# Kernel tuning notes

Measured on AMD Instinct MI355X. Metric: run time of the kernel, lower is better.

Reference implementation:

```python
import jax, jax.numpy as jnp
import numpy as np

NEG_INF = -1e30  # mask value used by QANet's apply_mask


def setup_inputs() -> dict:
    key = jax.random.key(0)
    ks = jax.random.split(key, 6)
    B, C, Q, H = 64, 1024, 128, 512
    return {
        "x_context": jax.random.normal(ks[0], (B, C, H), dtype=jnp.float32),
        "x_query": jax.random.normal(ks[1], (B, Q, H), dtype=jnp.float32),
        "context_mask": jnp.ones((B, C), dtype=jnp.float32),
        "query_mask": jnp.ones((B, Q), dtype=jnp.float32),
        "W0": jax.random.normal(ks[2], (H,), dtype=jnp.float32) * 0.05,
        "W1": jax.random.normal(ks[3], (H,), dtype=jnp.float32) * 0.05,
        "W2": jax.random.normal(ks[4], (H,), dtype=jnp.float32) * 0.05,
        "bias": jnp.zeros((1,), dtype=jnp.float32),
    }


def reference(x_context, x_query, context_mask, query_mask, W0, W1, W2, bias):
    # Trilinear similarity S[b,c,q] = q.W0 + c.W1 + (q*W2).c + bias
    # (original computes [B,Q,C] then transposes; we build [B,C,Q] directly)
    sub0 = jnp.einsum('bqh,h->bq', x_query, W0)          # [B,Q]
    sub1 = jnp.einsum('bch,h->bc', x_context, W1)        # [B,C]
    sub2 = jnp.einsum('bch,bqh->bcq', x_context, x_query * W2)  # [B,C,Q]
    S = sub2 + sub1[:, :, None] + sub0[:, None, :] + bias  # [B,C,Q]

    mq = query_mask[:, None, :]    # [B,1,Q]
    mc = context_mask[:, :, None]  # [B,C,1]

    # context-to-query: softmax over query axis, masked by query_mask
    S_ = jax.nn.softmax(S + (1.0 - mq) * NEG_INF, axis=-1)  # [B,C,Q]
    c2q = jnp.einsum('bcq,bqh->bch', S_, x_query)           # [B,C,H]

    # query-to-context: softmax over context axis, masked by context_mask
    S_c = jax.nn.softmax(S + (1.0 - mc) * NEG_INF, axis=1)  # [B,C,Q]
    S_T = jnp.swapaxes(S_c, 1, 2)                            # [B,Q,C]
    # (S_ @ S_T) @ x_context, associated as S_ @ (S_T @ x_context)
    tmp = jnp.einsum('bqc,bch->bqh', S_T, x_context)        # [B,Q,H]
    q2c = jnp.einsum('bcq,bqh->bch', S_, tmp)               # [B,C,H]
    return c2q, q2c
```

## Files before the change

kernel.cpp:

```cpp
#include <hip/hip_runtime.h>

#define BB 64
#define CC 1024
#define QQ 128
#define HH 512

typedef short bf16x8 __attribute__((ext_vector_type(8)));
typedef float f32x4 __attribute__((ext_vector_type(4)));

#define GLD16(g, l)                                                            \
    __builtin_amdgcn_global_load_lds(                                          \
        (const __attribute__((address_space(1))) unsigned int*)(g),            \
        (__attribute__((address_space(3))) unsigned int*)(l), 16, 0, 0)

__device__ __forceinline__ unsigned short f2bf(float f) {
    unsigned u = __float_as_uint(f);
    u += 0x7FFF + ((u >> 16) & 1);
    return (unsigned short)(u >> 16);
}
__device__ __forceinline__ unsigned pk2(float lo, float hi) {
    return (unsigned)f2bf(lo) | ((unsigned)f2bf(hi) << 16);
}

__device__ __forceinline__ unsigned xcd_swz(unsigned orig, unsigned nwg) {
    return (orig & 7u) * (nwg >> 3) + (orig >> 3);
}

__global__ __launch_bounds__(256) void k_sub0(const float* __restrict__ xq,
                                              const float* __restrict__ w0,
                                              float* __restrict__ sub0,
                                              float* __restrict__ colsum) {
    if (blockIdx.x < 32) colsum[blockIdx.x * 256 + threadIdx.x] = 0.0f;
    int wave = threadIdx.x >> 6;
    int lane = threadIdx.x & 63;
    int row  = blockIdx.x * 4 + wave;
    const float* p = xq + (size_t)row * HH + lane * 8;
    float4 a0 = *(const float4*)(p);
    float4 a1 = *(const float4*)(p + 4);
    float4 b0 = *(const float4*)(w0 + lane * 8);
    float4 b1 = *(const float4*)(w0 + lane * 8 + 4);
    float s = a0.x*b0.x + a0.y*b0.y + a0.z*b0.z + a0.w*b0.w
            + a1.x*b1.x + a1.y*b1.y + a1.z*b1.z + a1.w*b1.w;
    #pragma unroll
    for (int off = 32; off; off >>= 1) s += __shfl_xor(s, off);
    if (lane == 0) sub0[row] = s;
}

__global__ __launch_bounds__(256) void k_prep(const float* __restrict__ xq,
                                              const float* __restrict__ w2,
                                              const float* __restrict__ qmask,
                                              unsigned short* __restrict__ xqw2b,
                                              unsigned short* __restrict__ xqmT) {
    int b  = blockIdx.y;
    int ht = blockIdx.x * 128;
    int tid = threadIdx.x;
    __shared__ __align__(16) unsigned short sT[128][132];

    {
        int q  = tid >> 1;
        int hh = (tid & 1) * 64;
        float qm = qmask[b * QQ + q];
        const float* xp = xq + ((size_t)b * QQ + q) * HH + ht + hh;
        unsigned short* wr = xqw2b + ((size_t)b * QQ + q) * HH + ht + hh;
        #pragma unroll
        for (int i = 0; i < 16; i++) {
            float4 v = *(const float4*)(xp + i * 4);
            float4 w = *(const float4*)(w2 + ht + hh + i * 4);
            uint2 pw; pw.x = pk2(v.x * w.x, v.y * w.y);
                      pw.y = pk2(v.z * w.z, v.w * w.w);
            *(uint2*)(wr + i * 4) = pw;
            uint2 pm; pm.x = pk2(v.x * qm, v.y * qm);
                      pm.y = pk2(v.z * qm, v.w * qm);
            *(uint2*)(&sT[q][hh + i * 4]) = pm;
        }
    }
    __syncthreads();
    {
        int h  = tid >> 1;
        int qh = (tid & 1) * 64;
        unsigned short* orow = xqmT + ((size_t)b * HH + ht + h) * QQ + qh;
        #pragma unroll
        for (int i = 0; i < 8; i++) {
            uint4 o;
            o.x = (unsigned)sT[qh + i*8 + 0][h] | ((unsigned)sT[qh + i*8 + 1][h] << 16);
            o.y = (unsigned)sT[qh + i*8 + 2][h] | ((unsigned)sT[qh + i*8 + 3][h] << 16);
            o.z = (unsigned)sT[qh + i*8 + 4][h] | ((unsigned)sT[qh + i*8 + 5][h] << 16);
            o.w = (unsigned)sT[qh + i*8 + 6][h] | ((unsigned)sT[qh + i*8 + 7][h] << 16);
            *(uint4*)(orow + i * 8) = o;
        }
    }
}

__global__ __launch_bounds__(256) void k_scores(
    const float* __restrict__ xc, const unsigned short* __restrict__ xqw2b,
    const float* __restrict__ w1, const float* __restrict__ cmask,
    const float* __restrict__ qmask, const float* __restrict__ bias,
    const float* __restrict__ sub0, unsigned short* __restrict__ Ebf,
    float* __restrict__ rowsum, float* __restrict__ colsum) {
    unsigned swz = xcd_swz(blockIdx.x, CC / 64 * BB);
    int b  = swz >> 4;
    int c0 = (swz & 15) * 64;
    int tid  = threadIdx.x;
    int lane = tid & 63, wave = tid >> 6;
    int quad = lane >> 4, lcol = lane & 15;
    int wrow = (wave >> 1) * 32, wcol = (wave & 1) * 64;

    __shared__ __align__(16) unsigned short sA[2][64][32];
    __shared__ __align__(16) unsigned short sB[2][128][32];
    __shared__ float sW1[512];
    __shared__ float sSub1[64];
    __shared__ float sS0[128], sQm[128], sCm[64];
    __shared__ float sRowP[2][64], sColP[2][128];

    sW1[tid] = w1[tid]; sW1[tid + 256] = w1[tid + 256];
    if (tid < 128) {
        sS0[tid] = sub0[b * QQ + tid] + bias[0];
        sQm[tid] = qmask[b * QQ + tid];
    }
    if (tid < 64) sCm[tid] = cmask[b * CC + c0 + tid];

    f32x4 acc[2][4];
    #pragma unroll
    for (int i = 0; i < 2; i++)
        #pragma unroll
        for (int j = 0; j < 4; j++) acc[i][j] = (f32x4)0.0f;
    float s1 = 0.0f;

    int arow = tid >> 2, akh = (tid & 3) * 8;
    const float* gbase = xc + ((size_t)(b * CC + c0 + arow)) * HH + akh;

    __syncthreads();

    {
        float4 v0 = *(const float4*)(gbase);
        float4 v1 = *(const float4*)(gbase + 4);
        const float* wp = sW1 + akh;
        s1 += v0.x*wp[0] + v0.y*wp[1] + v0.z*wp[2] + v0.w*wp[3]
            + v1.x*wp[4] + v1.y*wp[5] + v1.z*wp[6] + v1.w*wp[7];
        uint4 p;
        p.x = pk2(v0.x, v0.y); p.y = pk2(v0.z, v0.w);
        p.z = pk2(v1.x, v1.y); p.w = pk2(v1.z, v1.w);
        *(uint4*)&sA[0][arow][akh] = p;
    }
    #pragma unroll
    for (int j = 0; j < 2; j++) {
        int chunk = wave * 2 + j;
        int row = chunk * 16 + (lane >> 2);
        GLD16(xqw2b + ((size_t)b * QQ + row) * HH + (lane & 3) * 8,
              (unsigned short*)sB[0] + chunk * 512);
    }
    __syncthreads();

    for (int t = 0; t < 16; ++t) {
        int cur = t & 1, alt = cur ^ 1;
        bool pf = (t < 15);
        int kn = (t + 1) * 32;
        float4 v0, v1;
        if (pf) {
            const float* gp = gbase + kn;
            v0 = *(const float4*)(gp);
            v1 = *(const float4*)(gp + 4);
            #pragma unroll
            for (int j = 0; j < 2; j++) {
                int chunk = wave * 2 + j;
                int row = chunk * 16 + (lane >> 2);
                GLD16(xqw2b + ((size_t)b * QQ + row) * HH + kn + (lane & 3) * 8,
                      (unsigned short*)sB[alt] + chunk * 512);
            }
        }
        bf16x8 af[2];
        #pragma unroll
        for (int mi = 0; mi < 2; mi++)
            af[mi] = *(const bf16x8*)&sA[cur][wrow + mi * 16 + lcol][quad * 8];
        #pragma unroll
        for (int ni = 0; ni < 4; ni++) {
            bf16x8 bfr = *(const bf16x8*)&sB[cur][wcol + ni * 16 + lcol][quad * 8];
            #pragma unroll
            for (int mi = 0; mi < 2; mi++)
                acc[mi][ni] = __builtin_amdgcn_mfma_f32_16x16x32_bf16(
                    af[mi], bfr, acc[mi][ni], 0, 0, 0);
        }
        if (pf) {
            const float* wp = sW1 + kn + akh;
            s1 += v0.x*wp[0] + v0.y*wp[1] + v0.z*wp[2] + v0.w*wp[3]
                + v1.x*wp[4] + v1.y*wp[5] + v1.z*wp[6] + v1.w*wp[7];
            uint4 p;
            p.x = pk2(v0.x, v0.y); p.y = pk2(v0.z, v0.w);
            p.z = pk2(v1.x, v1.y); p.w = pk2(v1.z, v1.w);
            *(uint4*)&sA[alt][arow][akh] = p;
        }
        __syncthreads();
    }

    s1 += __shfl_xor(s1, 1);
    s1 += __shfl_xor(s1, 2);
    if ((tid & 3) == 0) sSub1[arow] = s1;
    __syncthreads();

    float rsp[2][4];
    float csp[4] = {0.f, 0.f, 0.f, 0.f};
    #pragma unroll
    for (int mi = 0; mi < 2; mi++)
        #pragma unroll
        for (int r = 0; r < 4; r++) rsp[mi][r] = 0.f;

    #pragma unroll
    for (int mi = 0; mi < 2; mi++) {
        #pragma unroll
        for (int ni = 0; ni < 4; ni++) {
            int col = wcol + ni * 16 + lcol;
            float qm = sQm[col], s0 = sS0[col];
            #pragma unroll
            for (int r = 0; r < 4; r++) {
                int row = wrow + mi * 16 + quad * 4 + r;
                float e = __expf(acc[mi][ni][r] + sSub1[row] + s0);
                acc[mi][ni][r] = e;
                rsp[mi][r] += e * qm;
                csp[ni] += e * sCm[row];
            }
        }
    }
    #pragma unroll
    for (int mi = 0; mi < 2; mi++)
        #pragma unroll
        for (int r = 0; r < 4; r++) {
            float v = rsp[mi][r];
            v += __shfl_xor(v, 1); v += __shfl_xor(v, 2);
            v += __shfl_xor(v, 4); v += __shfl_xor(v, 8);
            if (lcol == 0) sRowP[wave & 1][wrow + mi * 16 + quad * 4 + r] = v;
        }
    #pragma unroll
    for (int ni = 0; ni < 4; ni++) {
        float v = csp[ni];
        v += __shfl_xor(v, 16); v += __shfl_xor(v, 32);
        if (quad == 0) sColP[wave >> 1][wcol + ni * 16 + lcol] = v;
    }
    #pragma unroll
    for (int mi = 0; mi < 2; mi++)
        #pragma unroll
        for (int ni = 0; ni < 4; ni++) {
            int col = wcol + ni * 16 + lcol;
            #pragma unroll
            for (int r = 0; r < 4; r++) {
                int row = wrow + mi * 16 + quad * 4 + r;
                Ebf[((size_t)(b * CC + c0 + row)) * QQ + col] = f2bf(acc[mi][ni][r]);
            }
        }
    __syncthreads();
    if (tid < 64)
        rowsum[(size_t)b * CC + c0 + tid] = sRowP[0][tid] + sRowP[1][tid];
    if (tid < 128)
        atomicAdd(&colsum[b * QQ + tid], sColP[0][tid] + sColP[1][tid]);
}

__global__ __launch_bounds__(256) void k_tmp(
    const unsigned short* __restrict__ Ebf, const float* __restrict__ xc,
    const float* __restrict__ cmask, const float* __restrict__ qmask,
    const float* __restrict__ colsum, unsigned short* __restrict__ tmpT) {
    unsigned swz = xcd_swz(blockIdx.x, HH / 64 * BB);
    int b  = swz >> 3;
    int h0 = (swz & 7) * 64;
    int tid  = threadIdx.x;
    int lane = tid & 63, wave = tid >> 6;
    int quad = lane >> 4, lcol = lane & 15;
    int wrow = (wave >> 1) * 64;
    int wcol = (wave & 1) * 32;

    __shared__ __align__(16) unsigned int sAu[2][128 * 16];
    __shared__ __align__(16) unsigned int sBu[2][64 * 16];
    __shared__ float sInv[128];
    if (tid < 128) sInv[tid] = qmask[b * QQ + tid] / colsum[b * QQ + tid];

    f32x4 acc[4][2];
    #pragma unroll
    for (int i = 0; i < 4; i++) { acc[i][0] = (f32x4)0.f; acc[i][1] = (f32x4)0.f; }

    int tp = tid >> 4;
    int tq = tid & 15;

    const unsigned short* ebase = Ebf + ((size_t)b * CC + 2 * tp) * QQ + tq * 8;
    const float*          xbase = xc  + ((size_t)b * CC + 2 * tp) * HH + h0 + tq * 4;
    const float*          mbase = cmask + (size_t)b * CC + 2 * tp;

    {
        union { uint4 v; unsigned short s[8]; } r0, r1;
        r0.v = *(const uint4*)(ebase);
        r1.v = *(const uint4*)(ebase + QQ);
        float cm0 = mbase[0];
        float cm1 = mbase[1];
        float4 f0 = *(const float4*)(xbase);
        float4 f1 = *(const float4*)(xbase + HH);
        #pragma unroll
        for (int j = 0; j < 8; j++) {
            int q = tq * 8 + j;
            unsigned pk = (unsigned)r0.s[j] | ((unsigned)r1.s[j] << 16);
            sAu[0][q * 16 + (((tp >> 2) ^ (q >> 3 & 3)) << 2) + (tp & 3)] = pk;
        }
        float a0[4] = {f0.x, f0.y, f0.z, f0.w};
        float a1[4] = {f1.x, f1.y, f1.z, f1.w};
        #pragma unroll
        for (int j = 0; j < 4; j++) {
            int h = tq * 4 + j;
            unsigned pk = pk2(a0[j] * cm0, a1[j] * cm1);
            sBu[0][h * 16 + (((tp >> 2) ^ (h >> 3 & 3)) << 2) + (tp & 3)] = pk;
        }
    }
    __syncthreads();

    for (int t = 0; t < 32; ++t) {
        int cur = t & 1, alt = cur ^ 1;
        bool pf = (t < 31);
        int cn = (t + 1) * 32;
        union { uint4 v; unsigned short s[8]; } r0, r1;
        float4 f0, f1;
        float cm0, cm1;
        if (pf) {
            r0.v = *(const uint4*)(ebase + (size_t)cn * QQ);
            r1.v = *(const uint4*)(ebase + (size_t)cn * QQ + QQ);
            cm0 = mbase[cn];
            cm1 = mbase[cn + 1];
            f0 = *(const float4*)(xbase + (size_t)cn * HH);
            f1 = *(const float4*)(xbase + (size_t)cn * HH + HH);
        }
        bf16x8 af[4];
        #pragma unroll
        for (int mi = 0; mi < 4; mi++) {
            int m = wrow + mi * 16 + lcol;
            af[mi] = *(const bf16x8*)(sAu[cur] + m * 16 + ((quad ^ (m >> 3 & 3)) << 2));
        }
        #pragma unroll
        for (int ni = 0; ni < 2; ni++) {
            int n = wcol + ni * 16 + lcol;
            bf16x8 bfr = *(const bf16x8*)(sBu[cur] + n * 16 + ((quad ^ (n >> 3 & 3)) << 2));
            #pragma unroll
            for (int mi = 0; mi < 4; mi++)
                acc[mi][ni] = __builtin_amdgcn_mfma_f32_16x16x32_bf16(
                    af[mi], bfr, acc[mi][ni], 0, 0, 0);
        }
        if (pf) {
            #pragma unroll
            for (int j = 0; j < 8; j++) {
                int q = tq * 8 + j;
                unsigned pk = (unsigned)r0.s[j] | ((unsigned)r1.s[j] << 16);
                sAu[alt][q * 16 + (((tp >> 2) ^ (q >> 3 & 3)) << 2) + (tp & 3)] = pk;
            }
            float a0[4] = {f0.x, f0.y, f0.z, f0.w};
            float a1[4] = {f1.x, f1.y, f1.z, f1.w};
            #pragma unroll
            for (int j = 0; j < 4; j++) {
                int h = tq * 4 + j;
                unsigned pk = pk2(a0[j] * cm0, a1[j] * cm1);
                sBu[alt][h * 16 + (((tp >> 2) ^ (h >> 3 & 3)) << 2) + (tp & 3)] = pk;
            }
        }
        __syncthreads();
    }
    #pragma unroll
    for (int mi = 0; mi < 4; mi++) {
        int qb = wrow + mi * 16 + quad * 4;
        #pragma unroll
        for (int ni = 0; ni < 2; ni++) {
            int h = wcol + ni * 16 + lcol;
            uint2 o;
            o.x = pk2(acc[mi][ni][0] * sInv[qb + 0], acc[mi][ni][1] * sInv[qb + 1]);
            o.y = pk2(acc[mi][ni][2] * sInv[qb + 2], acc[mi][ni][3] * sInv[qb + 3]);
            *(uint2*)(tmpT + ((size_t)b * HH + h0 + h) * QQ + qb) = o;
        }
    }
}

__global__ __launch_bounds__(256) void k_out(
    const unsigned short* __restrict__ Ebf, const unsigned short* __restrict__ xqmT,
    const unsigned short* __restrict__ tmpT, const float* __restrict__ rowsum,
    float* __restrict__ c2q, float* __restrict__ q2c) {
    unsigned swz = xcd_swz(blockIdx.x, (HH / 128) * 2 * (CC / 128) * BB);
    int x  = swz & 7;
    int c0 = ((swz >> 3) & 7) * 128;
    int b  = swz >> 6;
    int which = x & 1;
    int h0 = (x >> 1) * 128;
    const unsigned short* Bsrc = which ? tmpT : xqmT;
    float* dst = which ? q2c : c2q;
    int tid  = threadIdx.x;
    int lane = tid & 63, wave = tid >> 6;
    int quad = lane >> 4, lcol = lane & 15;
    int wrow = (wave >> 1) * 64, wcol = (wave & 1) * 64;

    __shared__ __align__(16) unsigned short sA[2][128][32];
    __shared__ __align__(16) unsigned short sB[2][128][32];
    __shared__ float sInvR[128];
    if (tid < 128) sInvR[tid] = 1.0f / rowsum[(size_t)b * CC + c0 + tid];

    f32x4 acc[4][4];
    #pragma unroll
    for (int i = 0; i < 4; i++)
        #pragma unroll
        for (int j = 0; j < 4; j++) acc[i][j] = (f32x4)0.f;

    #pragma unroll
    for (int j = 0; j < 2; j++) {
        int chunk = wave * 2 + j;
        int row = chunk * 16 + (lane >> 2);
        int kb  = (lane & 3) * 8;
        GLD16(Ebf  + ((size_t)b * CC + c0 + row) * QQ + kb,
              (unsigned short*)sA[0] + chunk * 512);
        GLD16(Bsrc + ((size_t)b * HH + h0 + row) * QQ + kb,
              (unsigned short*)sB[0] + chunk * 512);
    }
    __syncthreads();

    for (int t = 0; t < 4; ++t) {
        int cur = t & 1, alt = cur ^ 1;
        bool pf = (t < 3);
        int kn = (t + 1) * 32;
        if (pf) {
            #pragma unroll
            for (int j = 0; j < 2; j++) {
                int chunk = wave * 2 + j;
                int row = chunk * 16 + (lane >> 2);
                int kb  = (lane & 3) * 8;
                GLD16(Ebf  + ((size_t)b * CC + c0 + row) * QQ + kn + kb,
                      (unsigned short*)sA[alt] + chunk * 512);
                GLD16(Bsrc + ((size_t)b * HH + h0 + row) * QQ + kn + kb,
                      (unsigned short*)sB[alt] + chunk * 512);
            }
        }
        bf16x8 af[4];
        #pragma unroll
        for (int mi = 0; mi < 4; mi++)
            af[mi] = *(const bf16x8*)&sA[cur][wrow + mi * 16 + lcol][quad * 8];
        #pragma unroll
        for (int ni = 0; ni < 4; ni++) {
            bf16x8 bfr = *(const bf16x8*)&sB[cur][wcol + ni * 16 + lcol][quad * 8];
            #pragma unroll
            for (int mi = 0; mi < 4; mi++)
                acc[mi][ni] = __builtin_amdgcn_mfma_f32_16x16x32_bf16(
                    af[mi], bfr, acc[mi][ni], 0, 0, 0);
        }
        __syncthreads();
    }
    #pragma unroll
    for (int mi = 0; mi < 4; mi++) {
        int rb = wrow + mi * 16 + quad * 4;
        float ir0 = sInvR[rb], ir1 = sInvR[rb + 1], ir2 = sInvR[rb + 2], ir3 = sInvR[rb + 3];
        #pragma unroll
        for (int ni = 0; ni < 4; ni++) {
            int col = h0 + wcol + ni * 16 + lcol;
            size_t o0 = ((size_t)b * CC + c0 + rb) * HH + col;
            dst[o0]          = acc[mi][ni][0] * ir0;
            dst[o0 + HH]     = acc[mi][ni][1] * ir1;
            dst[o0 + 2*HH]   = acc[mi][ni][2] * ir2;
            dst[o0 + 3*HH]   = acc[mi][ni][3] * ir3;
        }
    }
}

extern "C" void kernel_launch(void* const* d_in, const int* in_sizes, int n_in,
                              void* d_out, int out_size, void* d_ws, size_t ws_size,
                              hipStream_t stream) {
    const float* xc    = (const float*)d_in[0];
    const float* xq    = (const float*)d_in[1];
    const float* cmask = (const float*)d_in[2];
    const float* qmask = (const float*)d_in[3];
    const float* w0    = (const float*)d_in[4];
    const float* w1    = (const float*)d_in[5];
    const float* w2    = (const float*)d_in[6];
    const float* bias  = (const float*)d_in[7];

    float* out = (float*)d_out;
    float* c2q = out;
    float* q2c = out + (size_t)BB * CC * HH;

    unsigned short* Ebf   = (unsigned short*)d_ws;
    unsigned short* xqw2b = Ebf   + (size_t)BB * CC * QQ;
    unsigned short* xqmT  = xqw2b + (size_t)BB * QQ * HH;
    unsigned short* tmpT  = xqmT  + (size_t)BB * QQ * HH;
    float* rowsum = (float*)(tmpT + (size_t)BB * QQ * HH);
    float* colsum = rowsum + (size_t)BB * CC;
    float* sub0   = colsum + (size_t)BB * QQ;

    k_sub0  <<<dim3(BB * QQ / 4),                 256, 0, stream>>>(xq, w0, sub0, colsum);
    k_prep  <<<dim3(HH / 128, BB),                256, 0, stream>>>(xq, w2, qmask, xqw2b, xqmT);
    k_scores<<<dim3(CC / 64 * BB),                256, 0, stream>>>(xc, xqw2b, w1, cmask, qmask,
                                                                    bias, sub0, Ebf, rowsum, colsum);
    k_tmp   <<<dim3(HH / 64 * BB),                256, 0, stream>>>(Ebf, xc, cmask, qmask,
                                                                    colsum, tmpT);
    k_out   <<<dim3((HH / 128) * 2 * (CC / 128) * BB), 256, 0, stream>>>(Ebf, xqmT, tmpT,
                                                                          rowsum, c2q, q2c);
}
```

Before: 458.1 us.

## Cache masked bf16 context in scores kernel and fuse sub0 into prep

k_scores now also writes a bf16 copy of x_context pre-multiplied by the context mask. k_tmp reads this half-size buffer instead of re-reading fp32 x_context and the mask, which removes the conversion work there. The separate sub0 kernel is folded into k_prep using atomic adds, and colsum/sub0 are zeroed with a memset. The cost is an extra 64MB write in k_scores in exchange for a 128MB fp32 read dropping to a 64MB bf16 read, plus atomics in prep.

```diff
diff --git a/kernel.cpp b/kernel.cpp
--- a/kernel.cpp
+++ b/kernel.cpp
@@ -26,68 +26,46 @@
     return (orig & 7u) * (nwg >> 3) + (orig >> 3);
 }
 
-__global__ __launch_bounds__(256) void k_sub0(const float* __restrict__ xq,
+__global__ __launch_bounds__(256) void k_prep(const float* __restrict__ xq,
                                               const float* __restrict__ w0,
-                                              float* __restrict__ sub0,
-                                              float* __restrict__ colsum) {
-    if (blockIdx.x < 32) colsum[blockIdx.x * 256 + threadIdx.x] = 0.0f;
-    int wave = threadIdx.x >> 6;
-    int lane = threadIdx.x & 63;
-    int row  = blockIdx.x * 4 + wave;
-    const float* p = xq + (size_t)row * HH + lane * 8;
-    float4 a0 = *(const float4*)(p);
-    float4 a1 = *(const float4*)(p + 4);
-    float4 b0 = *(const float4*)(w0 + lane * 8);
-    float4 b1 = *(const float4*)(w0 + lane * 8 + 4);
-    float s = a0.x*b0.x + a0.y*b0.y + a0.z*b0.z + a0.w*b0.w
-            + a1.x*b1.x + a1.y*b1.y + a1.z*b1.z + a1.w*b1.w;
-    #pragma unroll
-    for (int off = 32; off; off >>= 1) s += __shfl_xor(s, off);
-    if (lane == 0) sub0[row] = s;
-}
-
-__global__ __launch_bounds__(256) void k_prep(const float* __restrict__ xq,
                                               const float* __restrict__ w2,
                                               const float* __restrict__ qmask,
                                               unsigned short* __restrict__ xqw2b,
-                                              unsigned short* __restrict__ xqmT) {
+                                              unsigned short* __restrict__ xqmT,
+                                              float* __restrict__ sub0) {
     int b  = blockIdx.y;
     int ht = blockIdx.x * 128;
     int tid = threadIdx.x;
-    __shared__ __align__(16) unsigned short sT[128][132];
-
-    {
-        int q  = tid >> 1;
-        int hh = (tid & 1) * 64;
-        float qm = qmask[b * QQ + q];
-        const float* xp = xq + ((size_t)b * QQ + q) * HH + ht + hh;
-        unsigned short* wr = xqw2b + ((size_t)b * QQ + q) * HH + ht + hh;
-        #pragma unroll
-        for (int i = 0; i < 16; i++) {
-            float4 v = *(const float4*)(xp + i * 4);
-            float4 w = *(const float4*)(w2 + ht + hh + i * 4);
-            uint2 pw; pw.x = pk2(v.x * w.x, v.y * w.y);
-                      pw.y = pk2(v.z * w.z, v.w * w.w);
-            *(uint2*)(wr + i * 4) = pw;
-            uint2 pm; pm.x = pk2(v.x * qm, v.y * qm);
-                      pm.y = pk2(v.z * qm, v.w * qm);
-            *(uint2*)(&sT[q][hh + i * 4]) = pm;
-        }
-    }
-    __syncthreads();
-    {
-        int h  = tid >> 1;
-        int qh = (tid & 1) * 64;
-        unsigned short* orow = xqmT + ((size_t)b * HH + ht + h) * QQ + qh;
-        #pragma unroll
-        for (int i = 0; i < 8; i++) {
-            uint4 o;
-            o.x = (unsigned)sT[qh + i*8 + 0][h] | ((unsigned)sT[qh + i*8 + 1][h] << 16);
-            o.y = (unsigned)sT[qh + i*8 + 2][h] | ((unsigned)sT[qh + i*8 + 3][h] << 16);
-            o.z = (unsigned)sT[qh + i*8 + 4][h] | ((unsigned)sT[qh + i*8 + 5][h] << 16);
-            o.w = (unsigned)sT[qh + i*8 + 6][h] | ((unsigned)sT[qh + i*8 + 7][h] << 16);
-            *(uint4*)(orow + i * 8) = o;
-        }
+    int wave = tid >> 6, lane = tid & 63;
+    __shared__ __align__(16) unsigned short sT[128][130];
+    __shared__ float sW0[128], sW2[128], sQm[128];
+
+    if (tid < 128) { sW0[tid] = w0[ht + tid]; sQm[tid] = qmask[b * QQ + tid]; }
+    else           { sW2[tid - 128] = w2[ht + tid - 128]; }
+    __syncthreads();
+
+    for (int it = 0; it < 32; ++it) {
+        int q = it * 4 + wave;
+        float2 v = *(const float2*)(xq + ((size_t)b * QQ + q) * HH + ht + lane * 2);
+        unsigned pw = pk2(v.x * sW2[lane * 2], v.y * sW2[lane * 2 + 1]);
+        *(unsigned*)(xqw2b + ((size_t)b * QQ + q) * HH + ht + lane * 2) = pw;
+        float qm = sQm[q];
+        *(unsigned*)(&sT[q][lane * 2]) = pk2(v.x * qm, v.y * qm);
+        float s = v.x * sW0[lane * 2] + v.y * sW0[lane * 2 + 1];
+        #pragma unroll
+        for (int off = 32; off; off >>= 1) s += __shfl_xor(s, off);
+        if (lane == 0) atomicAdd(&sub0[b * QQ + q], s);
+    }
+    __syncthreads();
+    for (int it = 0; it < 8; ++it) {
+        int h  = it * 16 + wave * 4 + (lane >> 4);
+        int tq = lane & 15;
+        uint4 o;
+        o.x = (unsigned)sT[tq*8 + 0][h] | ((unsigned)sT[tq*8 + 1][h] << 16);
+        o.y = (unsigned)sT[tq*8 + 2][h] | ((unsigned)sT[tq*8 + 3][h] << 16);
+        o.z = (unsigned)sT[tq*8 + 4][h] | ((unsigned)sT[tq*8 + 5][h] << 16);
+        o.w = (unsigned)sT[tq*8 + 6][h] | ((unsigned)sT[tq*8 + 7][h] << 16);
+        *(uint4*)(xqmT + ((size_t)b * HH + ht + h) * QQ + tq * 8) = o;
     }
 }
 
@@ -96,6 +74,7 @@
     const float* __restrict__ w1, const float* __restrict__ cmask,
     const float* __restrict__ qmask, const float* __restrict__ bias,
     const float* __restrict__ sub0, unsigned short* __restrict__ Ebf,
+    unsigned short* __restrict__ xcmb,
     float* __restrict__ rowsum, float* __restrict__ colsum) {
     unsigned swz = xcd_swz(blockIdx.x, CC / 64 * BB);
     int b  = swz >> 4;
@@ -128,6 +107,7 @@
 
     int arow = tid >> 2, akh = (tid & 3) * 8;
     const float* gbase = xc + ((size_t)(b * CC + c0 + arow)) * HH + akh;
+    unsigned short* mbout = xcmb + ((size_t)(b * CC + c0 + arow)) * HH + akh;
 
     __syncthreads();
 
@@ -141,6 +121,11 @@
         p.x = pk2(v0.x, v0.y); p.y = pk2(v0.z, v0.w);
         p.z = pk2(v1.x, v1.y); p.w = pk2(v1.z, v1.w);
         *(uint4*)&sA[0][arow][akh] = p;
+        float cm = sCm[arow];
+        uint4 pm;
+        pm.x = pk2(v0.x*cm, v0.y*cm); pm.y = pk2(v0.z*cm, v0.w*cm);
+        pm.z = pk2(v1.x*cm, v1.y*cm); pm.w = pk2(v1.z*cm, v1.w*cm);
+        *(uint4*)(mbout) = pm;
     }
     #pragma unroll
     for (int j = 0; j < 2; j++) {
@@ -188,6 +173,11 @@
             p.x = pk2(v0.x, v0.y); p.y = pk2(v0.z, v0.w);
             p.z = pk2(v1.x, v1.y); p.w = pk2(v1.z, v1.w);
             *(uint4*)&sA[alt][arow][akh] = p;
+            float cm = sCm[arow];
+            uint4 pm;
+            pm.x = pk2(v0.x*cm, v0.y*cm); pm.y = pk2(v0.z*cm, v0.w*cm);
+            pm.z = pk2(v1.x*cm, v1.y*cm); pm.w = pk2(v1.z*cm, v1.w*cm);
+            *(uint4*)(mbout + kn) = pm;
         }
         __syncthreads();
     }
@@ -254,8 +244,8 @@
 }
 
 __global__ __launch_bounds__(256) void k_tmp(
-    const unsigned short* __restrict__ Ebf, const float* __restrict__ xc,
-    const float* __restrict__ cmask, const float* __restrict__ qmask,
+    const unsigned short* __restrict__ Ebf, const unsigned short* __restrict__ xcmb,
+    const float* __restrict__ qmask,
     const float* __restrict__ colsum, unsigned short* __restrict__ tmpT) {
     unsigned swz = xcd_swz(blockIdx.x, HH / 64 * BB);
     int b  = swz >> 3;
@@ -278,31 +268,30 @@
     int tp = tid >> 4;
     int tq = tid & 15;
 
-    const unsigned short* ebase = Ebf + ((size_t)b * CC + 2 * tp) * QQ + tq * 8;
-    const float*          xbase = xc  + ((size_t)b * CC + 2 * tp) * HH + h0 + tq * 4;
-    const float*          mbase = cmask + (size_t)b * CC + 2 * tp;
+    const unsigned short* ebase = Ebf  + ((size_t)b * CC + 2 * tp) * QQ + tq * 8;
+    const unsigned short* xbase = xcmb + ((size_t)b * CC + 2 * tp) * HH + h0 + tq * 4;
 
     {
         union { uint4 v; unsigned short s[8]; } r0, r1;
         r0.v = *(const uint4*)(ebase);
         r1.v = *(const uint4*)(ebase + QQ);
-        float cm0 = mbase[0];
-        float cm1 = mbase[1];
-        float4 f0 = *(const float4*)(xbase);
-        float4 f1 = *(const float4*)(xbase + HH);
+        uint2 u0 = *(const uint2*)(xbase);
+        uint2 u1 = *(const uint2*)(xbase + HH);
         #pragma unroll
         for (int j = 0; j < 8; j++) {
             int q = tq * 8 + j;
             unsigned pk = (unsigned)r0.s[j] | ((unsigned)r1.s[j] << 16);
             sAu[0][q * 16 + (((tp >> 2) ^ (q >> 3 & 3)) << 2) + (tp & 3)] = pk;
         }
-        float a0[4] = {f0.x, f0.y, f0.z, f0.w};
-        float a1[4] = {f1.x, f1.y, f1.z, f1.w};
+        unsigned pkh[4];
+        pkh[0] = (u0.x & 0xffffu) | (u1.x << 16);
+        pkh[1] = (u0.x >> 16)     | (u1.x & 0xffff0000u);
+        pkh[2] = (u0.y & 0xffffu) | (u1.y << 16);
+        pkh[3] = (u0.y >> 16)     | (u1.y & 0xffff0000u);
         #pragma unroll
         for (int j = 0; j < 4; j++) {
             int h = tq * 4 + j;
-            unsigned pk = pk2(a0[j] * cm0, a1[j] * cm1);
-            sBu[0][h * 16 + (((tp >> 2) ^ (h >> 3 & 3)) << 2) + (tp & 3)] = pk;
+            sBu[0][h * 16 + (((tp >> 2) ^ (h >> 3 & 3)) << 2) + (tp & 3)] = pkh[j];
         }
     }
     __syncthreads();
@@ -312,15 +301,12 @@
         bool pf = (t < 31);
         int cn = (t + 1) * 32;
         union { uint4 v; unsigned short s[8]; } r0, r1;
-        float4 f0, f1;
-        float cm0, cm1;
+        uint2 u0, u1;
         if (pf) {
             r0.v = *(const uint4*)(ebase + (size_t)cn * QQ);
             r1.v = *(const uint4*)(ebase + (size_t)cn * QQ + QQ);
-            cm0 = mbase[cn];
-            cm1 = mbase[cn + 1];
-            f0 = *(const float4*)(xbase + (size_t)cn * HH);
-            f1 = *(const float4*)(xbase + (size_t)cn * HH + HH);
+            u0 = *(const uint2*)(xbase + (size_t)cn * HH);
+            u1 = *(const uint2*)(xbase + (size_t)cn * HH + HH);
         }
         bf16x8 af[4];
         #pragma unroll
@@ -344,13 +330,15 @@
                 unsigned pk = (unsigned)r0.s[j] | ((unsigned)r1.s[j] << 16);
                 sAu[alt][q * 16 + (((tp >> 2) ^ (q >> 3 & 3)) << 2) + (tp & 3)] = pk;
             }
-            float a0[4] = {f0.x, f0.y, f0.z, f0.w};
-            float a1[4] = {f1.x, f1.y, f1.z, f1.w};
+            unsigned pkh[4];
+            pkh[0] = (u0.x & 0xffffu) | (u1.x << 16);
+            pkh[1] = (u0.x >> 16)     | (u1.x & 0xffff0000u);
+            pkh[2] = (u0.y & 0xffffu) | (u1.y << 16);
+            pkh[3] = (u0.y >> 16)     | (u1.y & 0xffff0000u);
             #pragma unroll
             for (int j = 0; j < 4; j++) {
                 int h = tq * 4 + j;
-                unsigned pk = pk2(a0[j] * cm0, a1[j] * cm1);
-                sBu[alt][h * 16 + (((tp >> 2) ^ (h >> 3 & 3)) << 2) + (tp & 3)] = pk;
+                sBu[alt][h * 16 + (((tp >> 2) ^ (h >> 3 & 3)) << 2) + (tp & 3)] = pkh[j];
             }
         }
         __syncthreads();
@@ -475,15 +463,19 @@
     unsigned short* xqw2b = Ebf   + (size_t)BB * CC * QQ;
     unsigned short* xqmT  = xqw2b + (size_t)BB * QQ * HH;
     unsigned short* tmpT  = xqmT  + (size_t)BB * QQ * HH;
-    float* rowsum = (float*)(tmpT + (size_t)BB * QQ * HH);
+    unsigned short* xcmb  = tmpT  + (size_t)BB * QQ * HH;
+    float* rowsum = (float*)(xcmb + (size_t)BB * CC * HH);
     float* colsum = rowsum + (size_t)BB * CC;
     float* sub0   = colsum + (size_t)BB * QQ;
 
-    k_sub0  <<<dim3(BB * QQ / 4),                 256, 0, stream>>>(xq, w0, sub0, colsum);
-    k_prep  <<<dim3(HH / 128, BB),                256, 0, stream>>>(xq, w2, qmask, xqw2b, xqmT);
+    hipMemsetAsync(colsum, 0, (size_t)BB * QQ * 2 * sizeof(float), stream);
+
+    k_prep  <<<dim3(HH / 128, BB),                256, 0, stream>>>(xq, w0, w2, qmask,
+                                                                    xqw2b, xqmT, sub0);
     k_scores<<<dim3(CC / 64 * BB),                256, 0, stream>>>(xc, xqw2b, w1, cmask, qmask,
-                                                                    bias, sub0, Ebf, rowsum, colsum);
-    k_tmp   <<<dim3(HH / 64 * BB),                256, 0, stream>>>(Ebf, xc, cmask, qmask,
+                                                                    bias, sub0, Ebf, xcmb,
+                                                                    rowsum, colsum);
+    k_tmp   <<<dim3(HH / 64 * BB),                256, 0, stream>>>(Ebf, xcmb, qmask,
                                                                     colsum, tmpT);
     k_out   <<<dim3((HH / 128) * 2 * (CC / 128) * BB), 256, 0, stream>>>(Ebf, xqmT, tmpT,
                                                                           rowsum, c2q, q2c);
```

Result: slower. 493.8 us (+7.8%).
